# Performance work log

Hardware: AMD Instinct MI355X
Metric: run time of the kernel (lower is better)

Reference implementation:

```python
import jax, jax.numpy as jnp
import numpy as np

N, E, D, S, H, L = 20000, 320000, 128, 16, 4, 64


def _ln(x, g, b):
    m = x.mean(-1, keepdims=True)
    v = jnp.mean((x - m) ** 2, -1, keepdims=True)
    return (x - m) / jnp.sqrt(v + 1e-6) * g + b


def _mlp3(x, w1, b1, g1, be1, w2, b2, g2, be2, w3, b3):
    h = jax.nn.silu(_ln(x @ w1 + b1, g1, be1))
    h = jax.nn.silu(_ln(h @ w2 + b2, g2, be2))
    return h @ w3 + b3


def _seg_softmax(a, idx, n):
    # torch_geometric.utils.softmax: per-destination-group stable softmax
    m = jax.ops.segment_max(a, idx, num_segments=n)
    m = jnp.where(jnp.isfinite(m), m, 0.0)
    e = jnp.exp(a - m[idx])
    s = jax.ops.segment_sum(e, idx, num_segments=n)
    return e / (s[idx] + 1e-16)


def setup_inputs() -> dict:
    key = jax.random.key(0)
    ks = jax.random.split(key, 32)
    rn = lambda k, sh, sc=1.0: jax.random.normal(k, sh, dtype=jnp.float32) * sc
    li = lambda k, fi, fo: rn(k, (fi, fo), 1.0 / np.sqrt(fi))
    z = lambda n_: jnp.zeros((n_,), jnp.float32)
    o = lambda n_: jnp.ones((n_,), jnp.float32)
    inp = {
        'node_in': rn(ks[0], (N, D)),
        'node_embed': rn(ks[1], (N, D)),
        'edge_sh': rn(ks[2], (E, S)),
        'edge_length_embedding': rn(ks[3], (E, L)),
        'edge_src': jax.random.randint(ks[4], (E,), 0, N, dtype=jnp.int32),
        'edge_dst': jax.random.randint(ks[5], (E,), 0, N, dtype=jnp.int32),
        'batch': jnp.zeros((N,), jnp.int32),
        'pre_lin_w': li(ks[6], 2 * D + L, D),
        'tp2_w1': li(ks[7], L, 64), 'tp2_b1': z(64),
        'tp2_w2': li(ks[8], 64, H * S), 'tp2_b2': z(H * S),
        'a_w1': li(ks[9], L, 64), 'a_b1': z(64), 'a_g1': o(64), 'a_be1': z(64),
        'a_w2': li(ks[10], 64, 64), 'a_b2': z(64), 'a_g2': o(64), 'a_be2': z(64),
        'a_w3': li(ks[11], 64, H), 'a_b3': z(H),
        'lin_w': li(ks[12], D * H, D),
        'lin_edge_w': li(ks[13], D * H, 64),
        's_w1': li(ks[14], 64, 64), 's_b1': z(64), 's_g1': o(64), 's_be1': z(64),
        's_w2': li(ks[15], 64, 64), 's_b2': z(64), 's_g2': o(64), 's_be2': z(64),
        's_w3': li(ks[16], 64, 32), 's_b3': z(32),
    }
    return inp


def reference(node_in, node_embed, edge_sh, edge_length_embedding, edge_src, edge_dst, batch,
              pre_lin_w, tp2_w1, tp2_b1, tp2_w2, tp2_b2,
              a_w1, a_b1, a_g1, a_be1, a_w2, a_b2, a_g2, a_be2, a_w3, a_b3,
              lin_w, lin_edge_w,
              s_w1, s_b1, s_g1, s_be1, s_w2, s_b2, s_g2, s_be2, s_w3, s_b3):
    e = edge_length_embedding.shape[0]
    n = node_in.shape[0]
    # gather + pre_lin
    msg = jnp.concatenate([node_in[edge_src], node_in[edge_dst], edge_length_embedding], -1) @ pre_lin_w  # [E,D]
    # EquiConv tp2: channelwise TP with radial-MLP per-edge per-(head,sh) weights
    radial = jax.nn.silu(edge_length_embedding @ tp2_w1 + tp2_b1) @ tp2_w2 + tp2_b2  # [E,H*S]
    scal = jnp.einsum('ehs,es->eh', radial.reshape(e, H, S), edge_sh)  # [E,H]
    value = msg[:, None, :] * scal[:, :, None]  # [E,H,D]
    alpha = _mlp3(edge_length_embedding, a_w1, a_b1, a_g1, a_be1, a_w2, a_b2, a_g2, a_be2, a_w3, a_b3)  # [E,H]
    edge_out = value * alpha[:, :, None]  # [E,H,D]
    edge_scalar = _mlp3(edge_out.reshape(e, -1) @ lin_edge_w,
                        s_w1, s_b1, s_g1, s_be1, s_w2, s_b2, s_g2, s_be2, s_w3, s_b3)  # [E,32]
    asm = _seg_softmax(alpha, edge_dst, n)  # [E,H]
    node_fea = jax.ops.segment_sum(value * asm[:, :, None], edge_dst, num_segments=n)  # [N,H,D]
    node_out = node_fea.reshape(n, -1) @ lin_w  # [N,D]
    return node_out, edge_scalar
```

## Files before the change

kernel.cpp:

```cpp
#include <hip/hip_runtime.h>

#define NN 20000
#define EE 320000
#define WTOT 27648

typedef unsigned short u16;
typedef unsigned int u32;
typedef __attribute__((ext_vector_type(8))) short bf16x8;
typedef __attribute__((ext_vector_type(8))) _Float16 f16x8;
typedef __attribute__((ext_vector_type(4))) float f32x4;

__device__ __forceinline__ float bf2f(u16 u){
  union { u32 i; float f; } v; v.i = ((u32)u) << 16; return v.f;
}
__device__ __forceinline__ u16 f2bf(float f){
  union { float f; u32 i; } v; v.f = f;
  u32 i = v.i;
  return (u16)((i + 0x7FFFu + ((i >> 16) & 1u)) >> 16);
}
__device__ __forceinline__ u32 pack2(float a, float b){
  return ((u32)f2bf(b) << 16) | (u32)f2bf(a);
}
__device__ __forceinline__ u16 f2h(float f){
  union { _Float16 h[2]; u32 u; } v; v.h[0] = (_Float16)f;
  return (u16)(v.u & 0xFFFF);
}

__global__ __launch_bounds__(256) void k_prep(
    const float* __restrict__ plw, const float* __restrict__ lew,
    const float* __restrict__ lw,
    u16* __restrict__ Bt1, u16* __restrict__ Bt2, u16* __restrict__ Bt3)
{
  int i = blockIdx.x * 256 + threadIdx.x;
  if (i < 128*320) {
    int n = i / 320, k = i % 320;
    Bt1[i] = f2bf(plw[k*128 + n]);
  }
  int j = i - 128*320;
  if (j >= 0 && j < 256*128) {
    int n = j / 128, k = j % 128;
    int h = n >> 6, c = n & 63;
    Bt2[j] = f2bf(lew[(h*128 + k)*64 + c]);
  }
  int l = i - 128*320 - 256*128;
  if (l >= 0 && l < 128*512) {
    int n = l / 512, k = l % 512;
    Bt3[l] = f2bf(lw[k*128 + n]);
  }
}

__global__ __launch_bounds__(256) void k_prep2(
    const float* __restrict__ aw1, const float* __restrict__ aw2, const float* __restrict__ aw3,
    const float* __restrict__ rw1, const float* __restrict__ rw2,
    const float* __restrict__ sw1, const float* __restrict__ sw2, const float* __restrict__ sw3,
    u16* __restrict__ W)
{
  int i = blockIdx.x * 256 + threadIdx.x;
  if (i >= WTOT) return;
  float v = 0.f;
  int j = i;
  if (j < 8192)      { int n = j >> 6, k = j & 63;
                       v = (n < 64) ? aw1[k*64 + n] : rw1[k*64 + (n - 64)]; }
  else if ((j -= 8192) < 4096) { int n = j >> 6, k = j & 63; v = aw2[k*64 + n]; }
  else if ((j -= 4096) < 1024) { int n = j >> 6, k = j & 63; v = (n < 4) ? aw3[k*4 + n] : 0.f; }
  else if ((j -= 1024) < 4096) { int n = j >> 6, k = j & 63; v = rw2[k*64 + n]; }
  else if ((j -= 4096) < 4096) { int n = j >> 6, k = j & 63; v = sw1[k*64 + n]; }
  else if ((j -= 4096) < 4096) { int n = j >> 6, k = j & 63; v = sw2[k*64 + n]; }
  else               { j -= 4096; int n = j >> 6, k = j & 63; v = sw3[k*32 + n]; }
  W[i] = f2h(v);
}

__global__ __launch_bounds__(256) void k_zero(int* __restrict__ counts){
  int i = blockIdx.x * 256 + threadIdx.x;
  if (i < NN) counts[i] = 0;
}
__global__ __launch_bounds__(256) void k_count(const int* __restrict__ edst, int* __restrict__ counts){
  int e = blockIdx.x * 256 + threadIdx.x;
  if (e < EE) atomicAdd(&counts[edst[e]], 1);
}
__global__ __launch_bounds__(1024) void k_scan(const int* __restrict__ counts,
                                               int* __restrict__ offs, int* __restrict__ cursor){
  __shared__ int part[1024];
  int t = threadIdx.x;
  int c0 = t * 20, c1 = c0 + 20; if (c1 > NN) c1 = NN; if (c0 > NN) c0 = NN;
  int s = 0;
  for (int i = c0; i < c1; ++i) s += counts[i];
  part[t] = s;
  __syncthreads();
  if (t == 0) {
    int run = 0;
    for (int i = 0; i < 1024; ++i) { int v = part[i]; part[i] = run; run += v; }
    offs[NN] = run;
  }
  __syncthreads();
  int run = part[t];
  for (int i = c0; i < c1; ++i) { offs[i] = run; cursor[i] = run; run += counts[i]; }
}
__global__ __launch_bounds__(256) void k_fill(const int* __restrict__ edst,
                                              int* __restrict__ cursor, int* __restrict__ eids){
  int e = blockIdx.x * 256 + threadIdx.x;
  if (e < EE) { int p = atomicAdd(&cursor[edst[e]], 1); eids[p] = e; }
}
__global__ __launch_bounds__(256) void k_sort(const int* __restrict__ offs, int* __restrict__ eids){
  int n = blockIdx.x * 256 + threadIdx.x;
  if (n >= NN) return;
  int b = offs[n], e = offs[n+1];
  for (int i = b + 1; i < e; ++i) {
    int v = eids[i]; int j = i - 1;
    while (j >= b && eids[j] > v) { eids[j+1] = eids[j]; --j; }
    eids[j+1] = v;
  }
}

template<int NI>
__device__ __forceinline__ void gemm16_lds(const u16 (*X)[72], int wrow, int lane,
                                           const u16* __restrict__ B, f32x4 acc[2][4])
{
  const int fr = lane & 15, fc = lane >> 4;
  #pragma unroll
  for (int mi = 0; mi < 2; ++mi)
    #pragma unroll
    for (int ni = 0; ni < NI; ++ni)
      acc[mi][ni] = (f32x4){0.f, 0.f, 0.f, 0.f};
  #pragma unroll
  for (int kk = 0; kk < 2; ++kk) {
    f16x8 a0 = *(const f16x8*)&X[wrow + fr][kk*32 + fc*8];
    f16x8 a1 = *(const f16x8*)&X[wrow + 16 + fr][kk*32 + fc*8];
    #pragma unroll
    for (int ni = 0; ni < NI; ++ni) {
      f16x8 b = *(const f16x8*)(B + (size_t)(ni*16 + fr)*64 + kk*32 + fc*8);
      acc[0][ni] = __builtin_amdgcn_mfma_f32_16x16x32_f16(a0, b, acc[0][ni], 0, 0, 0);
      acc[1][ni] = __builtin_amdgcn_mfma_f32_16x16x32_f16(a1, b, acc[1][ni], 0, 0, 0);
    }
  }
}

template<int NI>
__device__ __forceinline__ void gemm16_lds1(const u16 (*X)[72], int wrow, int lane,
                                            const u16* __restrict__ B, f32x4 acc[4])
{
  const int fr = lane & 15, fc = lane >> 4;
  #pragma unroll
  for (int ni = 0; ni < NI; ++ni) acc[ni] = (f32x4){0.f, 0.f, 0.f, 0.f};
  #pragma unroll
  for (int kk = 0; kk < 2; ++kk) {
    f16x8 a = *(const f16x8*)&X[wrow + fr][kk*32 + fc*8];
    #pragma unroll
    for (int ni = 0; ni < NI; ++ni) {
      f16x8 b = *(const f16x8*)(B + (size_t)(ni*16 + fr)*64 + kk*32 + fc*8);
      acc[ni] = __builtin_amdgcn_mfma_f32_16x16x32_f16(a, b, acc[ni], 0, 0, 0);
    }
  }
}

__device__ __forceinline__ void gemm32_glb8(const float* __restrict__ X, int row0, int lane,
                                            const u16* __restrict__ B, f32x4 acc[2][8])
{
  const int fr = lane & 15, fc = lane >> 4;
  #pragma unroll
  for (int mi = 0; mi < 2; ++mi)
    #pragma unroll
    for (int ni = 0; ni < 8; ++ni)
      acc[mi][ni] = (f32x4){0.f, 0.f, 0.f, 0.f};
  #pragma unroll
  for (int kk = 0; kk < 2; ++kk) {
    const float* p0 = X + (size_t)(row0 + fr)*64 + kk*32 + fc*8;
    const float* p1 = X + (size_t)(row0 + 16 + fr)*64 + kk*32 + fc*8;
    float4 v00 = ((const float4*)p0)[0], v01 = ((const float4*)p0)[1];
    float4 v10 = ((const float4*)p1)[0], v11 = ((const float4*)p1)[1];
    f16x8 a0, a1;
    a0[0]=(_Float16)v00.x; a0[1]=(_Float16)v00.y; a0[2]=(_Float16)v00.z; a0[3]=(_Float16)v00.w;
    a0[4]=(_Float16)v01.x; a0[5]=(_Float16)v01.y; a0[6]=(_Float16)v01.z; a0[7]=(_Float16)v01.w;
    a1[0]=(_Float16)v10.x; a1[1]=(_Float16)v10.y; a1[2]=(_Float16)v10.z; a1[3]=(_Float16)v10.w;
    a1[4]=(_Float16)v11.x; a1[5]=(_Float16)v11.y; a1[6]=(_Float16)v11.z; a1[7]=(_Float16)v11.w;
    #pragma unroll
    for (int ni = 0; ni < 8; ++ni) {
      f16x8 b = *(const f16x8*)(B + (size_t)(ni*16 + fr)*64 + kk*32 + fc*8);
      acc[0][ni] = __builtin_amdgcn_mfma_f32_16x16x32_f16(a0, b, acc[0][ni], 0, 0, 0);
      acc[1][ni] = __builtin_amdgcn_mfma_f32_16x16x32_f16(a1, b, acc[1][ni], 0, 0, 0);
    }
  }
}

template<bool LN>
__device__ __forceinline__ void act_store16(f32x4 acc[2][4],
    const float* __restrict__ b, const float* __restrict__ g, const float* __restrict__ be,
    u16 (*H)[72], int wrow, int lane)
{
  const int fr = lane & 15, fc = lane >> 4;
  float bv[4], gv[4], bev[4];
  #pragma unroll
  for (int ni = 0; ni < 4; ++ni) {
    bv[ni] = b[ni*16 + fr];
    if (LN) { gv[ni] = g[ni*16 + fr]; bev[ni] = be[ni*16 + fr]; }
  }
  #pragma unroll
  for (int mi = 0; mi < 2; ++mi)
    #pragma unroll
    for (int j = 0; j < 4; ++j) {
      int r = wrow + mi*16 + fc*4 + j;
      float x[4];
      #pragma unroll
      for (int ni = 0; ni < 4; ++ni) x[ni] = acc[mi][ni][j] + bv[ni];
      if (LN) {
        float s  = x[0] + x[1] + x[2] + x[3];
        float s2 = x[0]*x[0] + x[1]*x[1] + x[2]*x[2] + x[3]*x[3];
        #pragma unroll
        for (int off = 1; off < 16; off <<= 1) {
          s  += __shfl_xor(s,  off);
          s2 += __shfl_xor(s2, off);
        }
        float mu  = s * (1.f/64.f);
        float var = s2 * (1.f/64.f) - mu*mu;
        float rs  = rsqrtf(var + 1e-6f);
        #pragma unroll
        for (int ni = 0; ni < 4; ++ni) x[ni] = (x[ni] - mu)*rs*gv[ni] + bev[ni];
      }
      #pragma unroll
      for (int ni = 0; ni < 4; ++ni) {
        float y = x[ni];
        y = y / (1.f + __expf(-y));
        H[r][ni*16 + fr] = f2h(y);
      }
    }
}

template<bool LN>
__device__ __forceinline__ void act_store16_1(f32x4 acc[4],
    const float* __restrict__ b, const float* __restrict__ g, const float* __restrict__ be,
    u16 (*H)[72], int wrow, int lane)
{
  const int fr = lane & 15, fc = lane >> 4;
  float bv[4], gv[4], bev[4];
  #pragma unroll
  for (int ni = 0; ni < 4; ++ni) {
    bv[ni] = b[ni*16 + fr];
    if (LN) { gv[ni] = g[ni*16 + fr]; bev[ni] = be[ni*16 + fr]; }
  }
  #pragma unroll
  for (int j = 0; j < 4; ++j) {
    int r = wrow + fc*4 + j;
    float x[4];
    #pragma unroll
    for (int ni = 0; ni < 4; ++ni) x[ni] = acc[ni][j] + bv[ni];
    if (LN) {
      float s  = x[0] + x[1] + x[2] + x[3];
      float s2 = x[0]*x[0] + x[1]*x[1] + x[2]*x[2] + x[3]*x[3];
      #pragma unroll
      for (int off = 1; off < 16; off <<= 1) {
        s  += __shfl_xor(s,  off);
        s2 += __shfl_xor(s2, off);
      }
      float mu  = s * (1.f/64.f);
      float var = s2 * (1.f/64.f) - mu*mu;
      float rs  = rsqrtf(var + 1e-6f);
      #pragma unroll
      for (int ni = 0; ni < 4; ++ni) x[ni] = (x[ni] - mu)*rs*gv[ni] + bev[ni];
    }
    #pragma unroll
    for (int ni = 0; ni < 4; ++ni) {
      float y = x[ni];
      y = y / (1.f + __expf(-y));
      H[r][ni*16 + fr] = f2h(y);
    }
  }
}

__global__ __launch_bounds__(256, 4) void k_ar_mlp(
  const float* __restrict__ elen,
  const float* __restrict__ esh, const u16* __restrict__ Wm,
  const float* __restrict__ ab1, const float* __restrict__ ag1, const float* __restrict__ abe1,
  const float* __restrict__ ab2, const float* __restrict__ ag2, const float* __restrict__ abe2,
  const float* __restrict__ ab3,
  const float* __restrict__ tb1, const float* __restrict__ tb2,
  float* __restrict__ alpha_g, float* __restrict__ scal_g, float* __restrict__ cbuf_g)
{
  __shared__ u16 Ha[128][72], Hr[128][72];
  __shared__ float aS[128][4];
  const u16* Wc1 = Wm;
  const u16* Wa2 = Wm + 8192;
  const u16* Wa3 = Wm + 12288;
  const u16* Wr2 = Wm + 13312;
  const int tid = threadIdx.x;
  const int wave = tid >> 6, lane = tid & 63;
  const int fr = lane & 15, fc = lane >> 4;
  const int wrow = wave * 32;
  const int e0 = blockIdx.x * 128;
  {
    f32x4 acc8[2][8];
    gemm32_glb8(elen, e0 + wrow, lane, Wc1, acc8);
    float bva[4], gva[4], beva[4], bvr[4];
    #pragma unroll
    for (int ni = 0; ni < 4; ++ni) {
      bva[ni] = ab1[ni*16 + fr]; gva[ni] = ag1[ni*16 + fr]; beva[ni] = abe1[ni*16 + fr];
      bvr[ni] = tb1[ni*16 + fr];
    }
    #pragma unroll
    for (int mi = 0; mi < 2; ++mi)
      #pragma unroll
      for (int j = 0; j < 4; ++j) {
        int r = wrow + mi*16 + fc*4 + j;
        float xa[4], xr[4];
        #pragma unroll
        for (int ni = 0; ni < 4; ++ni) {
          xa[ni] = acc8[mi][ni][j] + bva[ni];
          xr[ni] = acc8[mi][ni+4][j] + bvr[ni];
        }
        float s  = xa[0] + xa[1] + xa[2] + xa[3];
        float s2 = xa[0]*xa[0] + xa[1]*xa[1] + xa[2]*xa[2] + xa[3]*xa[3];
        #pragma unroll
        for (int off = 1; off < 16; off <<= 1) {
          s  += __shfl_xor(s,  off);
          s2 += __shfl_xor(s2, off);
        }
        float mu  = s * (1.f/64.f);
        float var = s2 * (1.f/64.f) - mu*mu;
        float rs  = rsqrtf(var + 1e-6f);
        #pragma unroll
        for (int ni = 0; ni < 4; ++ni) {
          float y = (xa[ni] - mu)*rs*gva[ni] + beva[ni];
          y = y / (1.f + __expf(-y));
          Ha[r][ni*16 + fr] = f2h(y);
          float z = xr[ni];
          z = z / (1.f + __expf(-z));
          Hr[r][ni*16 + fr] = f2h(z);
        }
      }
  }
  f32x4 acc[2][4];
  gemm16_lds<4>(Ha, wrow, lane, Wa2, acc);
  act_store16<true>(acc, ab2, ag2, abe2, Ha, wrow, lane);
  gemm16_lds<1>(Ha, wrow, lane, Wa3, acc);
  {
    float bv = (fr < 4) ? ab3[fr] : 0.f;
    #pragma unroll
    for (int mi = 0; mi < 2; ++mi)
      #pragma unroll
      for (int j = 0; j < 4; ++j) {
        int r = wrow + mi*16 + fc*4 + j;
        float v = acc[mi][0][j] + bv;
        if (fr < 4) {
          alpha_g[(size_t)(e0 + r)*4 + fr] = v;
          aS[r][fr] = v;
        }
      }
  }
  gemm16_lds<4>(Hr, wrow, lane, Wr2, acc);
  {
    float bv[4];
    #pragma unroll
    for (int ni = 0; ni < 4; ++ni) bv[ni] = tb2[ni*16 + fr];
    #pragma unroll
    for (int mi = 0; mi < 2; ++mi)
      #pragma unroll
      for (int j = 0; j < 4; ++j) {
        int r = wrow + mi*16 + fc*4 + j;
        float shv = esh[(size_t)(e0 + r)*16 + fr];
        float sc[4];
        #pragma unroll
        for (int ni = 0; ni < 4; ++ni) {
          float t = (acc[mi][ni][j] + bv[ni]) * shv;
          #pragma unroll
          for (int off = 1; off < 16; off <<= 1) t += __shfl_xor(t, off);
          sc[ni] = t;
        }
        if (fr == 0) {
          float4 sv; sv.x = sc[0]; sv.y = sc[1]; sv.z = sc[2]; sv.w = sc[3];
          *(float4*)(scal_g + (size_t)(e0 + r)*4) = sv;
          float4 cv;
          cv.x = sc[0]*aS[r][0]; cv.y = sc[1]*aS[r][1];
          cv.z = sc[2]*aS[r][2]; cv.w = sc[3]*aS[r][3];
          *(float4*)(cbuf_g + (size_t)(e0 + r)*4) = cv;
        }
      }
  }
}

__global__ __launch_bounds__(256) void g1_msg(
    const float* __restrict__ node_in, const float* __restrict__ elen,
    const int* __restrict__ esrc, const int* __restrict__ edst,
    const u16* __restrict__ Bt1, u16* __restrict__ msgb)
{
  __shared__ u16 As[128][40];
  __shared__ u16 Bs[128][40];
  const int tid = threadIdx.x;
  const int e0 = blockIdx.x * 128;
  const int wave = tid >> 6, lane = tid & 63;
  const int wr = (wave >> 1) * 64, wc = (wave & 1) * 64;
  const int fr = lane & 15, fc = lane >> 4;
  f32x4 acc[4][4] = {};
  const int r = tid >> 1, half = tid & 1;
  const int e = e0 + r;
  const int s_idx = esrc[e], d_idx = edst[e];
  for (int k0 = 0; k0 < 320; k0 += 32) {
    const int kk = k0 + half * 16;
    const float* ap;
    if (kk < 128)      ap = node_in + (size_t)s_idx*128 + kk;
    else if (kk < 256) ap = node_in + (size_t)d_idx*128 + (kk - 128);
    else               ap = elen + (size_t)e*64 + (kk - 256);
    u32* asp = (u32*)&As[r][half*16];
    #pragma unroll
    for (int q = 0; q < 4; ++q) {
      float4 v = *(const float4*)(ap + q*4);
      asp[q*2]   = pack2(v.x, v.y);
      asp[q*2+1] = pack2(v.z, v.w);
    }
    const uint4* bp = (const uint4*)(Bt1 + (size_t)r*320 + kk);
    *(uint4*)&Bs[r][half*16]     = bp[0];
    *(uint4*)&Bs[r][half*16 + 8] = bp[1];
    __syncthreads();
    bf16x8 a[4], b[4];
    #pragma unroll
    for (int mi = 0; mi < 4; ++mi) a[mi] = *(const bf16x8*)&As[wr + mi*16 + fr][fc*8];
    #pragma unroll
    for (int ni = 0; ni < 4; ++ni) b[ni] = *(const bf16x8*)&Bs[wc + ni*16 + fr][fc*8];
    #pragma unroll
    for (int mi = 0; mi < 4; ++mi)
      #pragma unroll
      for (int ni = 0; ni < 4; ++ni)
        acc[mi][ni] = __builtin_amdgcn_mfma_f32_16x16x32_bf16(a[mi], b[ni], acc[mi][ni], 0, 0, 0);
    __syncthreads();
  }
  #pragma unroll
  for (int mi = 0; mi < 4; ++mi)
    #pragma unroll
    for (int j = 0; j < 4; ++j) {
      int row = wr + mi*16 + fc*4 + j;
      size_t base = (size_t)(e0 + row)*128 + wc + fr;
      #pragma unroll
      for (int ni = 0; ni < 4; ++ni)
        msgb[base + ni*16] = f2bf(acc[mi][ni][j]);
    }
}

union G2Smem {
  struct { u16 As[64][40]; u16 Bs[256][40]; } s;
  float R[2][64][66];
};
__global__ __launch_bounds__(256) void g2s(
    const u16* __restrict__ msgb, const u16* __restrict__ Bt2,
    const float* __restrict__ cbuf, const u16* __restrict__ Wm,
    const float* __restrict__ b1, const float* __restrict__ g1, const float* __restrict__ be1,
    const float* __restrict__ b2, const float* __restrict__ g2, const float* __restrict__ be2,
    const float* __restrict__ b3,
    float* __restrict__ oute)
{
  __shared__ G2Smem u;
  __shared__ float cS[64][4];
  __shared__ u16 X[64][72];
  const u16* Ws1 = Wm + 17408;
  const u16* Ws2 = Wm + 21504;
  const u16* Ws3 = Wm + 25600;
  const int tid = threadIdx.x, wave = tid >> 6, lane = tid & 63;
  const int e0 = blockIdx.x * 64;
  const int fr = lane & 15, fc = lane >> 4;
  cS[tid >> 2][tid & 3] = cbuf[(size_t)e0*4 + tid];
  f32x4 acc[4][4] = {};
  for (int k0 = 0; k0 < 128; k0 += 32) {
    {
      int r = tid >> 2, q = tid & 3;
      *(uint4*)&u.s.As[r][q*8] = *(const uint4*)(msgb + (size_t)(e0 + r)*128 + k0 + q*8);
    }
    {
      const uint4* bp = (const uint4*)(Bt2 + (size_t)tid*128 + k0);
      *(uint4*)&u.s.Bs[tid][0]  = bp[0];
      *(uint4*)&u.s.Bs[tid][8]  = bp[1];
      *(uint4*)&u.s.Bs[tid][16] = bp[2];
      *(uint4*)&u.s.Bs[tid][24] = bp[3];
    }
    __syncthreads();
    bf16x8 a[4], b[4];
    #pragma unroll
    for (int mi = 0; mi < 4; ++mi) a[mi] = *(const bf16x8*)&u.s.As[mi*16 + fr][fc*8];
    #pragma unroll
    for (int ni = 0; ni < 4; ++ni) b[ni] = *(const bf16x8*)&u.s.Bs[wave*64 + ni*16 + fr][fc*8];
    #pragma unroll
    for (int mi = 0; mi < 4; ++mi)
      #pragma unroll
      for (int ni = 0; ni < 4; ++ni)
        acc[mi][ni] = __builtin_amdgcn_mfma_f32_16x16x32_bf16(a[mi], b[ni], acc[mi][ni], 0, 0, 0);
    __syncthreads();
  }
  const int h = wave;
  if ((wave & 1) == 0) {
    float (*Rb)[66] = u.R[wave >> 1];
    #pragma unroll
    for (int mi = 0; mi < 4; ++mi)
      #pragma unroll
      for (int j = 0; j < 4; ++j) {
        int row = mi*16 + fc*4 + j;
        float cv = cS[row][h];
        #pragma unroll
        for (int ni = 0; ni < 4; ++ni)
          Rb[row][ni*16 + fr] = acc[mi][ni][j] * cv;
      }
  }
  __syncthreads();
  if (wave & 1) {
    float (*Rb)[66] = u.R[wave >> 1];
    #pragma unroll
    for (int mi = 0; mi < 4; ++mi)
      #pragma unroll
      for (int j = 0; j < 4; ++j) {
        int row = mi*16 + fc*4 + j;
        float cv = cS[row][h];
        #pragma unroll
        for (int ni = 0; ni < 4; ++ni)
          Rb[row][ni*16 + fr] += acc[mi][ni][j] * cv;
      }
  }
  __syncthreads();
  {
    int rr = tid >> 2, j0 = (tid & 3) * 16;
    #pragma unroll
    for (int i = 0; i < 16; ++i)
      X[rr][j0 + i] = f2h(u.R[0][rr][j0 + i] + u.R[1][rr][j0 + i]);
  }
  const int wrow = wave * 16;
  f32x4 sa[4];
  gemm16_lds1<4>(X, wrow, lane, Ws1, sa);
  act_store16_1<true>(sa, b1, g1, be1, X, wrow, lane);
  gemm16_lds1<4>(X, wrow, lane, Ws2, sa);
  act_store16_1<true>(sa, b2, g2, be2, X, wrow, lane);
  gemm16_lds1<2>(X, wrow, lane, Ws3, sa);
  {
    float bv[2];
    bv[0] = b3[fr]; bv[1] = b3[16 + fr];
    #pragma unroll
    for (int j = 0; j < 4; ++j) {
      int r = wrow + fc*4 + j;
      #pragma unroll
      for (int ni = 0; ni < 2; ++ni)
        oute[(size_t)(e0 + r)*32 + ni*16 + fr] = sa[ni][j] + bv[ni];
    }
  }
}

__global__ __launch_bounds__(256) void k_node(
  const int* __restrict__ offs, const int* __restrict__ eids,
  const float* __restrict__ alpha, const float* __restrict__ scal,
  const u16* __restrict__ msgb, u16* __restrict__ nfb)
{
  const int w = threadIdx.x >> 6, lane = threadIdx.x & 63;
  const int n = blockIdx.x * 4 + w;
  const int beg = offs[n], end = offs[n+1];
  float m0=-3e38f, m1=-3e38f, m2=-3e38f, m3=-3e38f;
  for (int i = beg + lane; i < end; i += 64) {
    int eid = eids[i];
    float4 a = *(const float4*)(alpha + (size_t)eid*4);
    m0 = fmaxf(m0, a.x); m1 = fmaxf(m1, a.y);
    m2 = fmaxf(m2, a.z); m3 = fmaxf(m3, a.w);
  }
  #pragma unroll
  for (int off = 1; off < 64; off <<= 1) {
    m0 = fmaxf(m0, __shfl_xor(m0, off));
    m1 = fmaxf(m1, __shfl_xor(m1, off));
    m2 = fmaxf(m2, __shfl_xor(m2, off));
    m3 = fmaxf(m3, __shfl_xor(m3, off));
  }
  float se0=0.f, se1=0.f, se2=0.f, se3=0.f;
  float f00=0.f, f01=0.f, f10=0.f, f11=0.f, f20=0.f, f21=0.f, f30=0.f, f31=0.f;
  for (int i = beg; i < end; ++i) {
    int eid = eids[i];
    float4 a = *(const float4*)(alpha + (size_t)eid*4);
    float4 s = *(const float4*)(scal + (size_t)eid*4);
    float e0 = __expf(a.x - m0), e1 = __expf(a.y - m1);
    float e2 = __expf(a.z - m2), e3 = __expf(a.w - m3);
    se0 += e0; se1 += e1; se2 += e2; se3 += e3;
    float w0 = e0*s.x, w1 = e1*s.y, w2 = e2*s.z, w3 = e3*s.w;
    float v0 = bf2f(msgb[(size_t)eid*128 + lane]);
    float v1 = bf2f(msgb[(size_t)eid*128 + 64 + lane]);
    f00 = fmaf(w0, v0, f00); f01 = fmaf(w0, v1, f01);
    f10 = fmaf(w1, v0, f10); f11 = fmaf(w1, v1, f11);
    f20 = fmaf(w2, v0, f20); f21 = fmaf(w2, v1, f21);
    f30 = fmaf(w3, v0, f30); f31 = fmaf(w3, v1, f31);
  }
  float i0 = 1.f/(se0 + 1e-16f), i1 = 1.f/(se1 + 1e-16f);
  float i2 = 1.f/(se2 + 1e-16f), i3 = 1.f/(se3 + 1e-16f);
  size_t b = (size_t)n * 512;
  nfb[b + 0*128 + lane]      = f2bf(f00*i0);
  nfb[b + 0*128 + 64 + lane] = f2bf(f01*i0);
  nfb[b + 1*128 + lane]      = f2bf(f10*i1);
  nfb[b + 1*128 + 64 + lane] = f2bf(f11*i1);
  nfb[b + 2*128 + lane]      = f2bf(f20*i2);
  nfb[b + 2*128 + 64 + lane] = f2bf(f21*i2);
  nfb[b + 3*128 + lane]      = f2bf(f30*i3);
  nfb[b + 3*128 + 64 + lane] = f2bf(f31*i3);
}

__global__ __launch_bounds__(256) void g10_out(
    const u16* __restrict__ nfb, const u16* __restrict__ Bt3,
    float* __restrict__ out)
{
  __shared__ u16 As[128][40];
  __shared__ u16 Bs[128][40];
  const int tid = threadIdx.x;
  const int n0 = blockIdx.x * 128;
  const int wave = tid >> 6, lane = tid & 63;
  const int wr = (wave >> 1) * 64, wc = (wave & 1) * 64;
  const int fr = lane & 15, fc = lane >> 4;
  f32x4 acc[4][4] = {};
  const int r = tid >> 1, half = tid & 1;
  const int n = n0 + r;
  for (int k0 = 0; k0 < 512; k0 += 32) {
    uint4 z; z.x=0; z.y=0; z.z=0; z.w=0;
    uint4 v0 = z, v1 = z;
    if (n < NN) {
      const uint4* apv = (const uint4*)(nfb + (size_t)n*512 + k0 + half*16);
      v0 = apv[0]; v1 = apv[1];
    }
    *(uint4*)&As[r][half*16]     = v0;
    *(uint4*)&As[r][half*16 + 8] = v1;
    const uint4* bp = (const uint4*)(Bt3 + (size_t)r*512 + k0 + half*16);
    *(uint4*)&Bs[r][half*16]     = bp[0];
    *(uint4*)&Bs[r][half*16 + 8] = bp[1];
    __syncthreads();
    bf16x8 a[4], b[4];
    #pragma unroll
    for (int mi = 0; mi < 4; ++mi) a[mi] = *(const bf16x8*)&As[wr + mi*16 + fr][fc*8];
    #pragma unroll
    for (int ni = 0; ni < 4; ++ni) b[ni] = *(const bf16x8*)&Bs[wc + ni*16 + fr][fc*8];
    #pragma unroll
    for (int mi = 0; mi < 4; ++mi)
      #pragma unroll
      for (int ni = 0; ni < 4; ++ni)
        acc[mi][ni] = __builtin_amdgcn_mfma_f32_16x16x32_bf16(a[mi], b[ni], acc[mi][ni], 0, 0, 0);
    __syncthreads();
  }
  #pragma unroll
  for (int mi = 0; mi < 4; ++mi)
    #pragma unroll
    for (int j = 0; j < 4; ++j) {
      int rowg = n0 + wr + mi*16 + fc*4 + j;
      if (rowg < NN) {
        size_t base = (size_t)rowg*128 + wc + fr;
        #pragma unroll
        for (int ni = 0; ni < 4; ++ni)
          out[base + ni*16] = acc[mi][ni][j];
      }
    }
}

extern "C" void kernel_launch(void* const* d_in, const int* in_sizes, int n_in,
                              void* d_out, int out_size, void* d_ws, size_t ws_size,
                              hipStream_t stream)
{
  const float* node_in    = (const float*)d_in[0];
  const float* edge_sh    = (const float*)d_in[2];
  const float* elen       = (const float*)d_in[3];
  const int*   esrc       = (const int*)d_in[4];
  const int*   edst       = (const int*)d_in[5];
  const float* pre_lin_w  = (const float*)d_in[7];
  const float* tp2_w1     = (const float*)d_in[8];
  const float* tp2_b1     = (const float*)d_in[9];
  const float* tp2_w2     = (const float*)d_in[10];
  const float* tp2_b2     = (const float*)d_in[11];
  const float* a_w1  = (const float*)d_in[12];
  const float* a_b1  = (const float*)d_in[13];
  const float* a_g1  = (const float*)d_in[14];
  const float* a_be1 = (const float*)d_in[15];
  const float* a_w2  = (const float*)d_in[16];
  const float* a_b2  = (const float*)d_in[17];
  const float* a_g2  = (const float*)d_in[18];
  const float* a_be2 = (const float*)d_in[19];
  const float* a_w3  = (const float*)d_in[20];
  const float* a_b3  = (const float*)d_in[21];
  const float* lin_w      = (const float*)d_in[22];
  const float* lin_edge_w = (const float*)d_in[23];
  const float* s_w1  = (const float*)d_in[24];
  const float* s_b1  = (const float*)d_in[25];
  const float* s_g1  = (const float*)d_in[26];
  const float* s_be1 = (const float*)d_in[27];
  const float* s_w2  = (const float*)d_in[28];
  const float* s_b2  = (const float*)d_in[29];
  const float* s_g2  = (const float*)d_in[30];
  const float* s_be2 = (const float*)d_in[31];
  const float* s_w3  = (const float*)d_in[32];
  const float* s_b3  = (const float*)d_in[33];

  float* out_node = (float*)d_out;
  float* out_edge = out_node + (size_t)NN * 128;

  char* ws = (char*)d_ws;
  size_t off = 0;
  auto take = [&](size_t bytes) -> char* {
    char* p = ws + off;
    off = (off + bytes + 255) & ~(size_t)255;
    return p;
  };
  u16*   msgb   = (u16*)take((size_t)EE * 128 * 2);
  u16*   nfb    = (u16*)take((size_t)NN * 512 * 2);
  float* alpha  = (float*)take((size_t)EE * 4 * 4);
  float* scal   = (float*)take((size_t)EE * 4 * 4);
  float* cbuf   = (float*)take((size_t)EE * 4 * 4);
  int*   counts = (int*)take((size_t)NN * 4);
  int*   offs   = (int*)take((size_t)(NN + 1) * 4);
  int*   cursor = (int*)take((size_t)NN * 4);
  int*   eids   = (int*)take((size_t)EE * 4);
  u16*   Bt1    = (u16*)take((size_t)128 * 320 * 2);
  u16*   Bt2    = (u16*)take((size_t)256 * 128 * 2);
  u16*   Bt3    = (u16*)take((size_t)128 * 512 * 2);
  u16*   Wmlp   = (u16*)take((size_t)WTOT * 2);

  k_prep<<<544, 256, 0, stream>>>(pre_lin_w, lin_edge_w, lin_w, Bt1, Bt2, Bt3);
  k_prep2<<<(WTOT + 255)/256, 256, 0, stream>>>(a_w1, a_w2, a_w3, tp2_w1, tp2_w2,
                                                s_w1, s_w2, s_w3, Wmlp);
  k_zero<<<(NN + 255)/256, 256, 0, stream>>>(counts);
  k_count<<<EE/256, 256, 0, stream>>>(edst, counts);
  k_scan<<<1, 1024, 0, stream>>>(counts, offs, cursor);
  k_fill<<<EE/256, 256, 0, stream>>>(edst, cursor, eids);
  k_sort<<<(NN + 255)/256, 256, 0, stream>>>(offs, eids);
  k_ar_mlp<<<EE/128, 256, 0, stream>>>(elen, edge_sh, Wmlp,
                                       a_b1, a_g1, a_be1, a_b2, a_g2, a_be2, a_b3,
                                       tp2_b1, tp2_b2, alpha, scal, cbuf);
  g1_msg<<<EE/128, 256, 0, stream>>>(node_in, elen, esrc, edst, Bt1, msgb);
  g2s<<<EE/64, 256, 0, stream>>>(msgb, Bt2, cbuf, Wmlp,
                                 s_b1, s_g1, s_be1, s_b2, s_g2, s_be2, s_b3, out_edge);
  k_node<<<NN/4, 256, 0, stream>>>(offs, eids, alpha, scal, msgb, nfb);
  g10_out<<<(NN + 127)/128, 256, 0, stream>>>(nfb, Bt3, out_node);
}
```

Measured before the change: 484.9 us.

## Repartition g2s GEMM so each wave owns full rows, reducing heads in registers

The first GEMM in the edge-scalar kernel is reorganised so each wave computes all 256 output columns (4 heads x 64) for its own 16 rows, rather than 64 rows for one head. The per-head scaling and head reduction then happen in registers, removing the float LDS staging buffer, two barriers and the cross-wave accumulation pass. LDS shrinks because X now overlays the GEMM staging buffers, and launch bounds request 4 blocks per CU. In exchange each wave issues more B-fragment LDS reads, since A fragments are no longer reused across column tiles.

Result: faster. 467.2 us (-3.7%).

```diff
diff --git a/kernel.cpp b/kernel.cpp
--- a/kernel.cpp
+++ b/kernel.cpp
@@ -435,9 +435,9 @@
 
 union G2Smem {
   struct { u16 As[64][40]; u16 Bs[256][40]; } s;
-  float R[2][64][66];
+  u16 X[64][72];
 };
-__global__ __launch_bounds__(256) void g2s(
+__global__ __launch_bounds__(256, 4) void g2s(
     const u16* __restrict__ msgb, const u16* __restrict__ Bt2,
     const float* __restrict__ cbuf, const u16* __restrict__ Wm,
     const float* __restrict__ b1, const float* __restrict__ g1, const float* __restrict__ be1,
@@ -447,15 +447,17 @@
 {
   __shared__ G2Smem u;
   __shared__ float cS[64][4];
-  __shared__ u16 X[64][72];
   const u16* Ws1 = Wm + 17408;
   const u16* Ws2 = Wm + 21504;
   const u16* Ws3 = Wm + 25600;
   const int tid = threadIdx.x, wave = tid >> 6, lane = tid & 63;
   const int e0 = blockIdx.x * 64;
   const int fr = lane & 15, fc = lane >> 4;
+  const int wrow = wave * 16;
   cS[tid >> 2][tid & 3] = cbuf[(size_t)e0*4 + tid];
-  f32x4 acc[4][4] = {};
+  f32x4 acc[16];
+  #pragma unroll
+  for (int ni = 0; ni < 16; ++ni) acc[ni] = (f32x4){0.f, 0.f, 0.f, 0.f};
   for (int k0 = 0; k0 < 128; k0 += 32) {
     {
       int r = tid >> 2, q = tid & 3;
@@ -469,60 +471,30 @@
       *(uint4*)&u.s.Bs[tid][24] = bp[3];
     }
     __syncthreads();
-    bf16x8 a[4], b[4];
-    #pragma unroll
-    for (int mi = 0; mi < 4; ++mi) a[mi] = *(const bf16x8*)&u.s.As[mi*16 + fr][fc*8];
-    #pragma unroll
-    for (int ni = 0; ni < 4; ++ni) b[ni] = *(const bf16x8*)&u.s.Bs[wave*64 + ni*16 + fr][fc*8];
-    #pragma unroll
-    for (int mi = 0; mi < 4; ++mi)
-      #pragma unroll
-      for (int ni = 0; ni < 4; ++ni)
-        acc[mi][ni] = __builtin_amdgcn_mfma_f32_16x16x32_bf16(a[mi], b[ni], acc[mi][ni], 0, 0, 0);
+    bf16x8 a = *(const bf16x8*)&u.s.As[wrow + fr][fc*8];
+    #pragma unroll
+    for (int ni = 0; ni < 16; ++ni) {
+      bf16x8 b = *(const bf16x8*)&u.s.Bs[ni*16 + fr][fc*8];
+      acc[ni] = __builtin_amdgcn_mfma_f32_16x16x32_bf16(a, b, acc[ni], 0, 0, 0);
+    }
     __syncthreads();
   }
-  const int h = wave;
-  if ((wave & 1) == 0) {
-    float (*Rb)[66] = u.R[wave >> 1];
-    #pragma unroll
-    for (int mi = 0; mi < 4; ++mi)
-      #pragma unroll
-      for (int j = 0; j < 4; ++j) {
-        int row = mi*16 + fc*4 + j;
-        float cv = cS[row][h];
-        #pragma unroll
-        for (int ni = 0; ni < 4; ++ni)
-          Rb[row][ni*16 + fr] = acc[mi][ni][j] * cv;
-      }
-  }
-  __syncthreads();
-  if (wave & 1) {
-    float (*Rb)[66] = u.R[wave >> 1];
-    #pragma unroll
-    for (int mi = 0; mi < 4; ++mi)
-      #pragma unroll
-      for (int j = 0; j < 4; ++j) {
-        int row = mi*16 + fc*4 + j;
-        float cv = cS[row][h];
-        #pragma unroll
-        for (int ni = 0; ni < 4; ++ni)
-          Rb[row][ni*16 + fr] += acc[mi][ni][j] * cv;
-      }
-  }
-  __syncthreads();
-  {
-    int rr = tid >> 2, j0 = (tid & 3) * 16;
-    #pragma unroll
-    for (int i = 0; i < 16; ++i)
-      X[rr][j0 + i] = f2h(u.R[0][rr][j0 + i] + u.R[1][rr][j0 + i]);
-  }
-  const int wrow = wave * 16;
+  #pragma unroll
+  for (int j = 0; j < 4; ++j) {
+    int r = wrow + fc*4 + j;
+    float c0 = cS[r][0], c1 = cS[r][1], c2 = cS[r][2], c3 = cS[r][3];
+    #pragma unroll
+    for (int m = 0; m < 4; ++m) {
+      float y = c0*acc[m][j] + c1*acc[4+m][j] + c2*acc[8+m][j] + c3*acc[12+m][j];
+      u.X[r][m*16 + fr] = f2h(y);
+    }
+  }
   f32x4 sa[4];
-  gemm16_lds1<4>(X, wrow, lane, Ws1, sa);
-  act_store16_1<true>(sa, b1, g1, be1, X, wrow, lane);
-  gemm16_lds1<4>(X, wrow, lane, Ws2, sa);
-  act_store16_1<true>(sa, b2, g2, be2, X, wrow, lane);
-  gemm16_lds1<2>(X, wrow, lane, Ws3, sa);
+  gemm16_lds1<4>(u.X, wrow, lane, Ws1, sa);
+  act_store16_1<true>(sa, b1, g1, be1, u.X, wrow, lane);
+  gemm16_lds1<4>(u.X, wrow, lane, Ws2, sa);
+  act_store16_1<true>(sa, b2, g2, be2, u.X, wrow, lane);
+  gemm16_lds1<2>(u.X, wrow, lane, Ws3, sa);
   {
     float bv[2];
     bv[0] = b3[fr]; bv[1] = b3[16 + fr];
```
